# Kernel optimization log

Measured on AMD Instinct MI355X. Metric: run time of the kernel, lower is better.

The kernel has to match this reference:

```python
import jax, jax.numpy as jnp
import numpy as np
import math

D_MODEL = 1024
NUM_HEADS = 16  # scale = sqrt(D_MODEL / NUM_HEADS)
BATCH, SEQ = 4, 4096


def setup_inputs() -> dict:
    key = jax.random.key(0)
    ks = jax.random.split(key, 7)
    s = 1.0 / math.sqrt(D_MODEL)
    return {
        "query": jax.random.normal(ks[0], (BATCH, SEQ, D_MODEL), jnp.float32),
        "value": jax.random.normal(ks[1], (BATCH, SEQ, D_MODEL), jnp.float32),
        "Wq": jax.random.normal(ks[2], (D_MODEL, D_MODEL), jnp.float32) * s,
        "bq": jax.random.normal(ks[3], (D_MODEL,), jnp.float32) * s,
        "qk_b": jnp.zeros((D_MODEL,), jnp.float32),
        "Wv": jax.random.normal(ks[4], (D_MODEL, D_MODEL), jnp.float32) * s,
        "bv": jax.random.normal(ks[5], (D_MODEL,), jnp.float32) * s,
    }


def reference(query, value, Wq, bq, qk_b, Wv, bv):
    # q_proj = Linear(query) + extra bias qk_b ; v_proj = Linear(value)
    q = jnp.einsum("bsd,ed->bse", query, Wq) + bq + qk_b   # [B,S,D]
    v = jnp.einsum("bsd,ed->bse", value, Wv) + bv          # [B,S,D]
    inv_scale = math.sqrt(query.shape[-1] / NUM_HEADS)
    scores = jnp.einsum("bqd,bkd->bqk", q, v) / inv_scale  # [B,S,S]
    attn = jax.nn.softmax(scores, axis=-1)
    # dropout_p = 0.0 -> identity
    return jnp.einsum("bqk,bkd->bqd", attn, v)             # [B,S,D]
```

## Files before the change

kernel.cpp:

```cpp
#include <hip/hip_runtime.h>

#define B_ 4
#define S_ 4096
#define D_ 1024

typedef __bf16 bf16;
typedef _Float16 f16;
typedef __attribute__((ext_vector_type(8))) __bf16 bf16x8;
typedef __attribute__((ext_vector_type(8))) _Float16 f16x8;
typedef __attribute__((ext_vector_type(4))) float floatx4;

__device__ inline floatx4 mfma16(bf16x8 a, bf16x8 b, floatx4 c) {
    return __builtin_amdgcn_mfma_f32_16x16x32_bf16(a, b, c, 0, 0, 0);
}
__device__ inline floatx4 mfma_any(bf16x8 a, bf16x8 b, floatx4 c) {
    return __builtin_amdgcn_mfma_f32_16x16x32_bf16(a, b, c, 0, 0, 0);
}
__device__ inline floatx4 mfma_any(f16x8 a, f16x8 b, floatx4 c) {
    return __builtin_amdgcn_mfma_f32_16x16x32_f16(a, b, c, 0, 0, 0);
}

template <typename T> struct vec8_of;
template <> struct vec8_of<bf16> { using type = bf16x8; };
template <> struct vec8_of<f16>  { using type = f16x8; };

__device__ inline bf16x8 cvt8(float4 a, float4 b) {
    bf16x8 h;
    h[0] = (bf16)a.x; h[1] = (bf16)a.y; h[2] = (bf16)a.z; h[3] = (bf16)a.w;
    h[4] = (bf16)b.x; h[5] = (bf16)b.y; h[6] = (bf16)b.z; h[7] = (bf16)b.w;
    return h;
}

__global__ __launch_bounds__(256) void cast_f32_bf16(
    const float* __restrict__ in, bf16* __restrict__ out)
{
    size_t i = ((size_t)blockIdx.x * 256 + threadIdx.x) * 8;
    float4 a = *(const float4*)(in + i);
    float4 b = *(const float4*)(in + i + 4);
    *(bf16x8*)(out + i) = cvt8(a, b);
}

template <typename TI, typename TO, bool HAS_BIAS>
__global__ __launch_bounds__(512, 2) void gemm256(
    const TI* __restrict__ A, const TI* __restrict__ B, TO* __restrict__ C,
    int K, int ldc, size_t strideA, size_t strideB, size_t strideC,
    const float* __restrict__ bias1, const float* __restrict__ bias2,
    float scale, int tiles_n)
{
    using v8 = typename vec8_of<TI>::type;
    __shared__ __align__(16) TI sA[2][2][8192];
    __shared__ __align__(16) TI sB[2][2][8192];

    A += (size_t)blockIdx.z * strideA;
    B += (size_t)blockIdx.z * strideB;
    C += (size_t)blockIdx.z * strideC;

    const int tid = threadIdx.x;
    const int wave = tid >> 6, lane = tid & 63, quad = lane >> 4, l16 = lane & 15;
    const int wm = wave >> 2, wn = wave & 3;

    const int gx = gridDim.x;
    const int cpx = gx >> 3;
    const int lid = (blockIdx.x & 7) * cpx + (blockIdx.x >> 3);
    const int tm = lid / tiles_n, tn = lid - tm * tiles_n;
    const int m0 = tm * 256, n0 = tn * 256;

    int r_[2], c_[2];
#pragma unroll
    for (int j = 0; j < 2; j++) {
        int idx = j * 512 + tid;
        int dB = idx * 16;
        int L = dB ^ (((dB >> 7) & 7) << 4);
        r_[j] = L >> 7;
        c_[j] = (L & 127) >> 1;
    }
    const int NT = K >> 6;

    auto stageA = [&](int t, int half, int bufsel) {
#pragma unroll
        for (int j = 0; j < 2; j++) {
            int idx = j * 512 + tid;
            __builtin_amdgcn_global_load_lds(
                (const __attribute__((address_space(1))) void*)(
                    A + (size_t)(m0 + half * 128 + r_[j]) * K + t * 64 + c_[j]),
                (__attribute__((address_space(3))) void*)(sA[bufsel][half] + idx * 8),
                16, 0, 0);
        }
    };
    auto stageB = [&](int t, int half, int bufsel) {
#pragma unroll
        for (int j = 0; j < 2; j++) {
            int idx = j * 512 + tid;
            __builtin_amdgcn_global_load_lds(
                (const __attribute__((address_space(1))) void*)(
                    B + (size_t)(n0 + half * 128 + r_[j]) * K + t * 64 + c_[j]),
                (__attribute__((address_space(3))) void*)(sB[bufsel][half] + idx * 8),
                16, 0, 0);
        }
    };
    auto rdA = [&](int buf, int i, int q) -> v8 {
        int row = i * 16 + l16;
        int byte = (row * 128 + q * 64 + quad * 16) ^ ((row & 7) << 4);
        return *(const v8*)((const char*)(sA[buf][wm]) + byte);
    };
    auto rdB = [&](int buf, int j, int q) -> v8 {
        int row = (wn & 1) * 64 + j * 16 + l16;
        int byte = (row * 128 + q * 64 + quad * 16) ^ ((row & 7) << 4);
        return *(const v8*)((const char*)(sB[buf][wn >> 1]) + byte);
    };

    floatx4 acc[8][4];
#pragma unroll
    for (int i = 0; i < 8; i++)
#pragma unroll
        for (int j = 0; j < 4; j++) acc[i][j] = (floatx4)0.0f;

    {
        int t1 = (1 < NT) ? 1 : NT - 1;
        stageA(0, 0, 0); stageA(0, 1, 0);
        stageB(0, 0, 0); stageB(0, 1, 0);
        stageB(t1, 0, 1); stageB(t1, 1, 1);
        asm volatile("s_waitcnt vmcnt(4)" ::: "memory");
        __builtin_amdgcn_s_barrier();
    }

    v8 a[8], b0[4], b1[4];
    for (int t = 0; t < NT; t++) {
        const int buf = t & 1;
        const int tA = (t + 1 < NT) ? t + 1 : NT - 1;
        const int tB = (t + 2 < NT) ? t + 2 : NT - 1;

#pragma unroll
        for (int i = 0; i < 4; i++) { a[2 * i] = rdA(buf, i, 0); a[2 * i + 1] = rdA(buf, i, 1); }
#pragma unroll
        for (int j = 0; j < 2; j++) { b0[2 * j] = rdB(buf, j, 0); b0[2 * j + 1] = rdB(buf, j, 1); }
        stageA(tA, 0, buf ^ 1);
        __builtin_amdgcn_s_barrier();
        __builtin_amdgcn_s_setprio(1);
#pragma unroll
        for (int i = 0; i < 4; i++)
#pragma unroll
            for (int j = 0; j < 2; j++) {
                acc[i][j] = mfma_any(a[2 * i], b0[2 * j], acc[i][j]);
                acc[i][j] = mfma_any(a[2 * i + 1], b0[2 * j + 1], acc[i][j]);
            }
        __builtin_amdgcn_s_setprio(0);
        __builtin_amdgcn_s_barrier();

#pragma unroll
        for (int j = 0; j < 2; j++) { b1[2 * j] = rdB(buf, 2 + j, 0); b1[2 * j + 1] = rdB(buf, 2 + j, 1); }
        stageA(tA, 1, buf ^ 1);
        __builtin_amdgcn_s_barrier();
        __builtin_amdgcn_s_setprio(1);
#pragma unroll
        for (int i = 0; i < 4; i++)
#pragma unroll
            for (int j = 0; j < 2; j++) {
                acc[i][2 + j] = mfma_any(a[2 * i], b1[2 * j], acc[i][2 + j]);
                acc[i][2 + j] = mfma_any(a[2 * i + 1], b1[2 * j + 1], acc[i][2 + j]);
            }
        __builtin_amdgcn_s_setprio(0);
        __builtin_amdgcn_s_barrier();

#pragma unroll
        for (int i = 0; i < 4; i++) { a[2 * i] = rdA(buf, 4 + i, 0); a[2 * i + 1] = rdA(buf, 4 + i, 1); }
        stageB(tB, 0, buf);
        __builtin_amdgcn_s_barrier();
        __builtin_amdgcn_s_setprio(1);
#pragma unroll
        for (int i = 0; i < 4; i++)
#pragma unroll
            for (int j = 0; j < 2; j++) {
                acc[4 + i][2 + j] = mfma_any(a[2 * i], b1[2 * j], acc[4 + i][2 + j]);
                acc[4 + i][2 + j] = mfma_any(a[2 * i + 1], b1[2 * j + 1], acc[4 + i][2 + j]);
            }
        __builtin_amdgcn_s_setprio(0);
        __builtin_amdgcn_s_barrier();

        stageB(tB, 1, buf);
        asm volatile("s_waitcnt vmcnt(4)" ::: "memory");
        __builtin_amdgcn_s_barrier();
        __builtin_amdgcn_s_setprio(1);
#pragma unroll
        for (int i = 0; i < 4; i++)
#pragma unroll
            for (int j = 0; j < 2; j++) {
                acc[4 + i][j] = mfma_any(a[2 * i], b0[2 * j], acc[4 + i][j]);
                acc[4 + i][j] = mfma_any(a[2 * i + 1], b0[2 * j + 1], acc[4 + i][j]);
            }
        __builtin_amdgcn_s_setprio(0);
        __builtin_amdgcn_s_barrier();
    }

#pragma unroll
    for (int mf = 0; mf < 8; mf++)
#pragma unroll
        for (int nf = 0; nf < 4; nf++) {
            int col = n0 + wn * 64 + nf * 16 + l16;
            float badd = 0.0f;
            if (HAS_BIAS) {
                badd = bias1[col];
                if (bias2) badd += bias2[col];
            }
#pragma unroll
            for (int r = 0; r < 4; r++) {
                int row = m0 + wm * 128 + mf * 16 + quad * 4 + r;
                float v = acc[mf][nf][r];
                if (HAS_BIAS) v = (v + badd) * scale;
                C[(size_t)row * ldc + col] = (TO)v;
            }
        }
}

template <typename TI, typename TO, bool HAS_BIAS>
__global__ __launch_bounds__(256) void gemm128(
    const TI* __restrict__ A, const TI* __restrict__ B, TO* __restrict__ C,
    int K, int ldc, size_t strideA, size_t strideB, size_t strideC,
    const float* __restrict__ bias1, const float* __restrict__ bias2, float scale)
{
    using v8 = typename vec8_of<TI>::type;
    __shared__ TI sA[2 * 128 * 32];
    __shared__ TI sB[2 * 128 * 32];
    A += (size_t)blockIdx.z * strideA;
    B += (size_t)blockIdx.z * strideB;
    C += (size_t)blockIdx.z * strideC;

    const int tid = threadIdx.x;
    const int wave = tid >> 6, lane = tid & 63, quad = lane >> 4, l16 = lane & 15;
    const int m0 = blockIdx.x * 128, n0 = blockIdx.y * 128;
    const int wr = (wave >> 1) * 64, wc = (wave & 1) * 64;

    floatx4 acc[4][4];
#pragma unroll
    for (int i = 0; i < 4; i++)
#pragma unroll
        for (int j = 0; j < 4; j++) acc[i][j] = (floatx4)0.0f;

    for (int k0 = 0; k0 < K; k0 += 64) {
#pragma unroll
        for (int s = 0; s < 2; s++) {
#pragma unroll
            for (int j = 0; j < 2; j++) {
                int idx = j * 256 + tid;
                int r = idx >> 2, c = (idx & 3) * 8;
                __builtin_amdgcn_global_load_lds(
                    (const __attribute__((address_space(1))) void*)(A + (size_t)(m0 + r) * K + k0 + s * 32 + c),
                    (__attribute__((address_space(3))) void*)(sA + s * 4096 + idx * 8), 16, 0, 0);
                __builtin_amdgcn_global_load_lds(
                    (const __attribute__((address_space(1))) void*)(B + (size_t)(n0 + r) * K + k0 + s * 32 + c),
                    (__attribute__((address_space(3))) void*)(sB + s * 4096 + idx * 8), 16, 0, 0);
            }
        }
        __syncthreads();
#pragma unroll
        for (int s = 0; s < 2; s++) {
            v8 af[4], bfv[4];
#pragma unroll
            for (int i = 0; i < 4; i++) {
                af[i]  = *(const v8*)&sA[s * 4096 + (wr + i * 16 + l16) * 32 + quad * 8];
                bfv[i] = *(const v8*)&sB[s * 4096 + (wc + i * 16 + l16) * 32 + quad * 8];
            }
#pragma unroll
            for (int mf = 0; mf < 4; mf++)
#pragma unroll
                for (int nf = 0; nf < 4; nf++)
                    acc[mf][nf] = mfma_any(af[mf], bfv[nf], acc[mf][nf]);
        }
        __syncthreads();
    }

#pragma unroll
    for (int mf = 0; mf < 4; mf++)
#pragma unroll
        for (int nf = 0; nf < 4; nf++) {
            int col = n0 + wc + nf * 16 + l16;
            float badd = 0.0f;
            if (HAS_BIAS) {
                badd = bias1[col];
                if (bias2) badd += bias2[col];
            }
#pragma unroll
            for (int r = 0; r < 4; r++) {
                int row = m0 + wr + mf * 16 + quad * 4 + r;
                float v = acc[mf][nf][r];
                if (HAS_BIAS) v = (v + badd) * scale;
                C[(size_t)row * ldc + col] = (TO)v;
            }
        }
}

__global__ __launch_bounds__(256) void transpose_v(
    const bf16* __restrict__ vb, bf16* __restrict__ vtb)
{
    __shared__ bf16 tile[32][33];
    const int b = blockIdx.z;
    const int s0 = blockIdx.x * 32, d0 = blockIdx.y * 32;
    const int tr = threadIdx.x >> 5;
    const int tc = threadIdx.x & 31;
#pragma unroll
    for (int k = 0; k < 4; k++) {
        int r = tr + k * 8;
        tile[r][tc] = vb[((size_t)b * S_ + s0 + r) * D_ + d0 + tc];
    }
    __syncthreads();
#pragma unroll
    for (int k = 0; k < 4; k++) {
        int r = tr + k * 8;
        vtb[((size_t)b * D_ + d0 + r) * S_ + s0 + tc] = tile[tc][r];
    }
}

__global__ __launch_bounds__(256) void transpose_v_f16(
    const bf16* __restrict__ vb, f16* __restrict__ vtb)
{
    __shared__ bf16 tile[32][33];
    const int b = blockIdx.z;
    const int s0 = blockIdx.x * 32, d0 = blockIdx.y * 32;
    const int tr = threadIdx.x >> 5;
    const int tc = threadIdx.x & 31;
#pragma unroll
    for (int k = 0; k < 4; k++) {
        int r = tr + k * 8;
        tile[r][tc] = vb[((size_t)b * S_ + s0 + r) * D_ + d0 + tc];
    }
    __syncthreads();
#pragma unroll
    for (int k = 0; k < 4; k++) {
        int r = tr + k * 8;
        vtb[((size_t)b * D_ + d0 + r) * S_ + s0 + tc] = (f16)(float)tile[tc][r];
    }
}

__global__ __launch_bounds__(256) void softmax_inplace_f16(f16* __restrict__ Sc)
{
    f16* row = Sc + (size_t)blockIdx.x * S_;
    const int tid = threadIdx.x, wave = tid >> 6, lane = tid & 63;
    __shared__ float redm[4], redl[4];

    f16x8 a = *(const f16x8*)(row + tid * 16);
    f16x8 b = *(const f16x8*)(row + tid * 16 + 8);
    float v[16];
#pragma unroll
    for (int j = 0; j < 8; j++) { v[j] = (float)a[j]; v[8 + j] = (float)b[j]; }

    float m = -1e30f;
#pragma unroll
    for (int j = 0; j < 16; j++) m = fmaxf(m, v[j]);
#pragma unroll
    for (int off = 32; off; off >>= 1) m = fmaxf(m, __shfl_xor(m, off));
    if (lane == 0) redm[wave] = m;
    __syncthreads();
    m = fmaxf(fmaxf(redm[0], redm[1]), fmaxf(redm[2], redm[3]));

    float s = 0.0f;
#pragma unroll
    for (int j = 0; j < 16; j++) { v[j] = __expf(v[j] - m); s += v[j]; }
#pragma unroll
    for (int off = 32; off; off >>= 1) s += __shfl_xor(s, off);
    if (lane == 0) redl[wave] = s;
    __syncthreads();
    s = redl[0] + redl[1] + redl[2] + redl[3];
    float inv = 1.0f / s;

#pragma unroll
    for (int j = 0; j < 8; j++) { a[j] = (f16)(v[j] * inv); b[j] = (f16)(v[8 + j] * inv); }
    *(f16x8*)(row + tid * 16) = a;
    *(f16x8*)(row + tid * 16 + 8) = b;
}

__global__ __launch_bounds__(256) void softmax_row(
    const float* __restrict__ Sc, f16* __restrict__ P)
{
    const int q = blockIdx.x;
    const float* row = Sc + (size_t)q * S_;
    f16* prow = P + (size_t)q * S_;
    const int tid = threadIdx.x, wave = tid >> 6, lane = tid & 63;

    float4 v[4];
#pragma unroll
    for (int i = 0; i < 4; i++) v[i] = *(const float4*)(row + tid * 16 + i * 4);

    float m = -1e30f;
#pragma unroll
    for (int i = 0; i < 4; i++)
        m = fmaxf(m, fmaxf(fmaxf(v[i].x, v[i].y), fmaxf(v[i].z, v[i].w)));
#pragma unroll
    for (int off = 32; off; off >>= 1) m = fmaxf(m, __shfl_xor(m, off));
    __shared__ float redm[4], redl[4];
    if (lane == 0) redm[wave] = m;
    __syncthreads();
    m = fmaxf(fmaxf(redm[0], redm[1]), fmaxf(redm[2], redm[3]));

    float p[16];
    float s = 0.0f;
#pragma unroll
    for (int i = 0; i < 4; i++) {
        p[i * 4 + 0] = __expf(v[i].x - m);
        p[i * 4 + 1] = __expf(v[i].y - m);
        p[i * 4 + 2] = __expf(v[i].z - m);
        p[i * 4 + 3] = __expf(v[i].w - m);
        s += p[i * 4] + p[i * 4 + 1] + p[i * 4 + 2] + p[i * 4 + 3];
    }
#pragma unroll
    for (int off = 32; off; off >>= 1) s += __shfl_xor(s, off);
    if (lane == 0) redl[wave] = s;
    __syncthreads();
    s = redl[0] + redl[1] + redl[2] + redl[3];
    float inv = 1.0f / s;

    f16x8 o0, o1;
#pragma unroll
    for (int j = 0; j < 8; j++) {
        o0[j] = (f16)(p[j] * inv);
        o1[j] = (f16)(p[8 + j] * inv);
    }
    *(f16x8*)(prow + tid * 16) = o0;
    *(f16x8*)(prow + tid * 16 + 8) = o1;
}

#define SSTR 40
__global__ __launch_bounds__(256) void proj_gemm(
    const float* __restrict__ A, const float* __restrict__ W,
    const float* __restrict__ bias1, const float* __restrict__ bias2,
    bf16* __restrict__ C, float scale)
{
    __shared__ bf16 sA[64 * SSTR];
    __shared__ bf16 sB[64 * SSTR];
    const int tid = threadIdx.x;
    const int wave = tid >> 6, lane = tid & 63, quad = lane >> 4, l16 = lane & 15;
    const int m0 = blockIdx.x * 64, n0 = blockIdx.y * 64;
    const int wr = (wave >> 1) * 32, wc = (wave & 1) * 32;
    const int lr = tid >> 2;
    const int lc = (tid & 3) * 8;

    floatx4 acc[2][2];
#pragma unroll
    for (int i = 0; i < 2; i++)
#pragma unroll
        for (int j = 0; j < 2; j++) acc[i][j] = (floatx4)0.0f;

    for (int k0 = 0; k0 < 1024; k0 += 32) {
        const float* ga = A + (size_t)(m0 + lr) * 1024 + k0 + lc;
        const float* gw = W + (size_t)(n0 + lr) * 1024 + k0 + lc;
        float4 a0 = *(const float4*)ga;
        float4 a1 = *(const float4*)(ga + 4);
        float4 w0 = *(const float4*)gw;
        float4 w1 = *(const float4*)(gw + 4);
        *(bf16x8*)&sA[lr * SSTR + lc] = cvt8(a0, a1);
        *(bf16x8*)&sB[lr * SSTR + lc] = cvt8(w0, w1);
        __syncthreads();
        bf16x8 af[2], bfv[2];
        af[0]  = *(bf16x8*)&sA[(wr + l16) * SSTR + quad * 8];
        af[1]  = *(bf16x8*)&sA[(wr + 16 + l16) * SSTR + quad * 8];
        bfv[0] = *(bf16x8*)&sB[(wc + l16) * SSTR + quad * 8];
        bfv[1] = *(bf16x8*)&sB[(wc + 16 + l16) * SSTR + quad * 8];
#pragma unroll
        for (int mf = 0; mf < 2; mf++)
#pragma unroll
            for (int nf = 0; nf < 2; nf++)
                acc[mf][nf] = mfma16(af[mf], bfv[nf], acc[mf][nf]);
        __syncthreads();
    }
#pragma unroll
    for (int mf = 0; mf < 2; mf++)
#pragma unroll
        for (int nf = 0; nf < 2; nf++) {
            int col = n0 + wc + nf * 16 + l16;
            float bsum = bias1[col] + (bias2 ? bias2[col] : 0.0f);
#pragma unroll
            for (int r = 0; r < 4; r++) {
                int row = m0 + wr + mf * 16 + quad * 4 + r;
                C[(size_t)row * 1024 + col] = (bf16)((acc[mf][nf][r] + bsum) * scale);
            }
        }
}

#define BR 32
#define TK 64
#define DC 256
__global__ __launch_bounds__(256, 2) void flash_attn(
    const bf16* __restrict__ qb, const bf16* __restrict__ vb,
    const bf16* __restrict__ vtb, float* __restrict__ out)
{
    __shared__ float sPart[4][32][65];
    __shared__ bf16 sP[32][72];
    __shared__ float sM[32], sL[32], sAlpha[32];

    const int tid = threadIdx.x;
    const int wave = tid >> 6, lane = tid & 63, quad = lane >> 4, l16 = lane & 15;
    const int b = blockIdx.y, q0 = blockIdx.x * BR;

    bf16x8 qf[2][8];
#pragma unroll
    for (int mf = 0; mf < 2; mf++)
#pragma unroll
        for (int ks = 0; ks < 8; ks++) {
            int row = q0 + mf * 16 + l16;
            int col = wave * DC + ks * 32 + quad * 8;
            qf[mf][ks] = *(const bf16x8*)(qb + ((size_t)b * S_ + row) * D_ + col);
        }

    floatx4 o[2][16];
#pragma unroll
    for (int mf = 0; mf < 2; mf++)
#pragma unroll
        for (int nf = 0; nf < 16; nf++) o[mf][nf] = (floatx4)0.0f;

    if (tid < 32) { sM[tid] = -1e30f; sL[tid] = 0.0f; }
    __syncthreads();

    for (int kt = 0; kt < S_ / TK; kt++) {
        const int k0 = kt * TK;
        floatx4 sp[2][4];
#pragma unroll
        for (int mf = 0; mf < 2; mf++)
#pragma unroll
            for (int nf = 0; nf < 4; nf++) sp[mf][nf] = (floatx4)0.0f;
#pragma unroll
        for (int ks = 0; ks < 8; ks++) {
            int col = wave * DC + ks * 32 + quad * 8;
#pragma unroll
            for (int nf = 0; nf < 4; nf++) {
                int key = k0 + nf * 16 + l16;
                bf16x8 vf = *(const bf16x8*)(vb + ((size_t)b * S_ + key) * D_ + col);
                sp[0][nf] = mfma16(qf[0][ks], vf, sp[0][nf]);
                sp[1][nf] = mfma16(qf[1][ks], vf, sp[1][nf]);
            }
        }
#pragma unroll
        for (int mf = 0; mf < 2; mf++)
#pragma unroll
            for (int nf = 0; nf < 4; nf++)
#pragma unroll
                for (int r = 0; r < 4; r++)
                    sPart[wave][mf * 16 + quad * 4 + r][nf * 16 + l16] = sp[mf][nf][r];
        __syncthreads();

        {
            const int rr = tid >> 3, c0 = (tid & 7) * 8;
            float v[8];
            float mx = -1e30f;
#pragma unroll
            for (int j = 0; j < 8; j++) {
                v[j] = sPart[0][rr][c0 + j] + sPart[1][rr][c0 + j] +
                       sPart[2][rr][c0 + j] + sPart[3][rr][c0 + j];
                mx = fmaxf(mx, v[j]);
            }
            mx = fmaxf(mx, __shfl_xor(mx, 1));
            mx = fmaxf(mx, __shfl_xor(mx, 2));
            mx = fmaxf(mx, __shfl_xor(mx, 4));
            float m_old = sM[rr];
            float m_new = fmaxf(m_old, mx);
            float rsum = 0.0f;
#pragma unroll
            for (int j = 0; j < 8; j++) {
                float p = __expf(v[j] - m_new);
                sP[rr][c0 + j] = (bf16)p;
                rsum += p;
            }
            rsum += __shfl_xor(rsum, 1);
            rsum += __shfl_xor(rsum, 2);
            rsum += __shfl_xor(rsum, 4);
            if ((tid & 7) == 0) {
                float alpha = __expf(m_old - m_new);
                sAlpha[rr] = alpha;
                sM[rr] = m_new;
                sL[rr] = sL[rr] * alpha + rsum;
            }
        }
        __syncthreads();

        float al[2][4];
#pragma unroll
        for (int mf = 0; mf < 2; mf++)
#pragma unroll
            for (int r = 0; r < 4; r++) al[mf][r] = sAlpha[mf * 16 + quad * 4 + r];
#pragma unroll
        for (int mf = 0; mf < 2; mf++)
#pragma unroll
            for (int nf = 0; nf < 16; nf++)
#pragma unroll
                for (int r = 0; r < 4; r++) o[mf][nf][r] *= al[mf][r];

#pragma unroll
        for (int ks2 = 0; ks2 < 2; ks2++) {
            bf16x8 pA[2];
            pA[0] = *(bf16x8*)&sP[l16][ks2 * 32 + quad * 8];
            pA[1] = *(bf16x8*)&sP[16 + l16][ks2 * 32 + quad * 8];
            int key = k0 + ks2 * 32 + quad * 8;
#pragma unroll
            for (int nf = 0; nf < 16; nf++) {
                int d = wave * DC + nf * 16 + l16;
                bf16x8 vtf = *(const bf16x8*)(vtb + ((size_t)b * D_ + d) * S_ + key);
                o[0][nf] = mfma16(pA[0], vtf, o[0][nf]);
                o[1][nf] = mfma16(pA[1], vtf, o[1][nf]);
            }
        }
        __syncthreads();
    }

#pragma unroll
    for (int mf = 0; mf < 2; mf++) {
        float inv[4];
#pragma unroll
        for (int r = 0; r < 4; r++) inv[r] = 1.0f / sL[mf * 16 + quad * 4 + r];
#pragma unroll
        for (int nf = 0; nf < 16; nf++) {
            int d = wave * DC + nf * 16 + l16;
#pragma unroll
            for (int r = 0; r < 4; r++) {
                int row = q0 + mf * 16 + quad * 4 + r;
                out[((size_t)b * S_ + row) * D_ + d] = o[mf][nf][r] * inv[r];
            }
        }
    }
}

extern "C" void kernel_launch(void* const* d_in, const int* in_sizes, int n_in,
                              void* d_out, int out_size, void* d_ws, size_t ws_size,
                              hipStream_t stream) {
    const float* query = (const float*)d_in[0];
    const float* value = (const float*)d_in[1];
    const float* Wq    = (const float*)d_in[2];
    const float* bq    = (const float*)d_in[3];
    const float* qk_b  = (const float*)d_in[4];
    const float* Wv    = (const float*)d_in[5];
    const float* bv    = (const float*)d_in[6];
    float* out = (float*)d_out;

    const size_t SD = (size_t)S_ * D_;
    const size_t SS = (size_t)S_ * S_;
    const size_t MB = 1024 * 1024;

    char* w = (char*)d_ws;
    bf16* qb = (bf16*)w;
    bf16* vb = (bf16*)(w + 32 * MB);

    if (ws_size >= 224 * MB) {
        f16* vtb = (f16*)(w + 64 * MB);
        f16* Sc  = (f16*)(w + 96 * MB);
        bf16* qc  = (bf16*)(w + 96 * MB);
        bf16* vc  = (bf16*)(w + 128 * MB);
        bf16* wqc = (bf16*)(w + 160 * MB);
        bf16* wvc = (bf16*)(w + 163 * MB);

        cast_f32_bf16<<<(B_ * SD) / 2048, 256, 0, stream>>>(query, qc);
        cast_f32_bf16<<<(B_ * SD) / 2048, 256, 0, stream>>>(value, vc);
        cast_f32_bf16<<<((size_t)D_ * D_) / 2048, 256, 0, stream>>>(Wq, wqc);
        cast_f32_bf16<<<((size_t)D_ * D_) / 2048, 256, 0, stream>>>(Wv, wvc);

        gemm256<bf16, bf16, true><<<dim3(256, 1, 1), 512, 0, stream>>>(
            qc, wqc, qb, D_, D_, 0, 0, 0, bq, qk_b, 0.125f, 4);
        gemm256<bf16, bf16, true><<<dim3(256, 1, 1), 512, 0, stream>>>(
            vc, wvc, vb, D_, D_, 0, 0, 0, bv, nullptr, 1.0f, 4);

        transpose_v_f16<<<dim3(S_ / 32, D_ / 32, B_), 256, 0, stream>>>(vb, vtb);

        gemm256<bf16, f16, false><<<dim3(256, 1, B_), 512, 0, stream>>>(
            qb, vb, Sc, D_, S_, SD, SD, SS, nullptr, nullptr, 1.0f, 16);

        softmax_inplace_f16<<<B_ * S_, 256, 0, stream>>>(Sc);

        gemm256<f16, float, false><<<dim3(64, 1, B_), 512, 0, stream>>>(
            Sc, vtb, out, S_, D_, SS, (size_t)D_ * S_, SD, nullptr, nullptr, 1.0f, 4);
    } else if (ws_size >= 192 * MB) {
        f16*   vtb = (f16*)(w + 64 * MB);
        float* Sc  = (float*)(w + 96 * MB);
        f16*   Pn  = (f16*)(w + 160 * MB);
        bf16*  qc  = (bf16*)(w + 96 * MB);
        bf16*  vc  = (bf16*)(w + 128 * MB);
        bf16*  wqc = (bf16*)(w + 160 * MB);
        bf16*  wvc = (bf16*)(w + 163 * MB);

        cast_f32_bf16<<<(B_ * SD) / 2048, 256, 0, stream>>>(query, qc);
        cast_f32_bf16<<<(B_ * SD) / 2048, 256, 0, stream>>>(value, vc);
        cast_f32_bf16<<<((size_t)D_ * D_) / 2048, 256, 0, stream>>>(Wq, wqc);
        cast_f32_bf16<<<((size_t)D_ * D_) / 2048, 256, 0, stream>>>(Wv, wvc);

        gemm128<bf16, bf16, true><<<dim3(128, 8, 1), 256, 0, stream>>>(
            qc, wqc, qb, D_, D_, 0, 0, 0, bq, qk_b, 0.125f);
        gemm128<bf16, bf16, true><<<dim3(128, 8, 1), 256, 0, stream>>>(
            vc, wvc, vb, D_, D_, 0, 0, 0, bv, nullptr, 1.0f);

        transpose_v_f16<<<dim3(S_ / 32, D_ / 32, B_), 256, 0, stream>>>(vb, vtb);

        for (int b = 0; b < B_; b++) {
            gemm128<bf16, float, false><<<dim3(32, 32, 1), 256, 0, stream>>>(
                qb + b * SD, vb + b * SD, Sc, D_, S_, 0, 0, 0, nullptr, nullptr, 1.0f);
            softmax_row<<<S_, 256, 0, stream>>>(Sc, Pn);
            gemm128<f16, float, false><<<dim3(32, 8, 1), 256, 0, stream>>>(
                Pn, vtb + (size_t)b * D_ * S_, out + b * SD, S_, D_,
                0, 0, 0, nullptr, nullptr, 1.0f);
        }
    } else {
        bf16* vtb = (bf16*)(w + 64 * MB);
        dim3 pg(16384 / 64, 1024 / 64);
        proj_gemm<<<pg, 256, 0, stream>>>(query, Wq, bq, qk_b, qb, 0.125f);
        proj_gemm<<<pg, 256, 0, stream>>>(value, Wv, bv, nullptr, vb, 1.0f);
        transpose_v<<<dim3(S_ / 32, D_ / 32, B_), 256, 0, stream>>>(vb, vtb);
        flash_attn<<<dim3(S_ / BR, B_), 256, 0, stream>>>(qb, vb, vtb, out);
    }
}
```

Measured before the change: 587.2 us.

## Restructure GEMM mainloop to prefetch next-tile fragments and group tiles 4x4

Reorders the 256x256 GEMM main loop so that A and B fragments for the next K-tile are read from shared memory while the current tile's MFMAs run. A is now staged two tiles ahead and B one tile ahead, with separate register sets (A0/A1, BP/BC) and adjusted vmcnt waits. It also remaps block IDs into 4x4 super-tiles for better L2 reuse and precomputes global base offsets to cut address arithmetic. The extra fragment registers raise register pressure, and the finer wait counts make correctness depend on precise load ordering.

```diff
diff --git a/kernel.cpp b/kernel.cpp
--- a/kernel.cpp
+++ b/kernel.cpp
@@ -62,19 +62,27 @@
     const int gx = gridDim.x;
     const int cpx = gx >> 3;
     const int lid = (blockIdx.x & 7) * cpx + (blockIdx.x >> 3);
-    const int tm = lid / tiles_n, tn = lid - tm * tiles_n;
+    const int p = lid >> 4, w = lid & 15;
+    const int pr = tiles_n >> 2;
+    const int Pm = p / pr, Pn = p - Pm * pr;
+    const int tm = Pm * 4 + (w >> 2), tn = Pn * 4 + (w & 3);
     const int m0 = tm * 256, n0 = tn * 256;
 
-    int r_[2], c_[2];
+    const TI* Abase = A + (size_t)m0 * K;
+    const TI* Bbase = B + (size_t)n0 * K;
+
+    size_t goff[2];
 #pragma unroll
     for (int j = 0; j < 2; j++) {
         int idx = j * 512 + tid;
         int dB = idx * 16;
         int L = dB ^ (((dB >> 7) & 7) << 4);
-        r_[j] = L >> 7;
-        c_[j] = (L & 127) >> 1;
+        int r = L >> 7;
+        int c = (L & 127) >> 1;
+        goff[j] = (size_t)r * K + c;
     }
     const int NT = K >> 6;
+    const size_t halfA = (size_t)128 * K;
 
     auto stageA = [&](int t, int half, int bufsel) {
 #pragma unroll
@@ -82,7 +90,7 @@
             int idx = j * 512 + tid;
             __builtin_amdgcn_global_load_lds(
                 (const __attribute__((address_space(1))) void*)(
-                    A + (size_t)(m0 + half * 128 + r_[j]) * K + t * 64 + c_[j]),
+                    Abase + (size_t)t * 64 + (half ? halfA : 0) + goff[j]),
                 (__attribute__((address_space(3))) void*)(sA[bufsel][half] + idx * 8),
                 16, 0, 0);
         }
@@ -93,7 +101,7 @@
             int idx = j * 512 + tid;
             __builtin_amdgcn_global_load_lds(
                 (const __attribute__((address_space(1))) void*)(
-                    B + (size_t)(n0 + half * 128 + r_[j]) * K + t * 64 + c_[j]),
+                    Bbase + (size_t)t * 64 + (half ? halfA : 0) + goff[j]),
                 (__attribute__((address_space(3))) void*)(sB[bufsel][half] + idx * 8),
                 16, 0, 0);
         }
@@ -119,74 +127,80 @@
         int t1 = (1 < NT) ? 1 : NT - 1;
         stageA(0, 0, 0); stageA(0, 1, 0);
         stageB(0, 0, 0); stageB(0, 1, 0);
-        stageB(t1, 0, 1); stageB(t1, 1, 1);
+        stageA(t1, 0, 1); stageA(t1, 1, 1);
         asm volatile("s_waitcnt vmcnt(4)" ::: "memory");
         __builtin_amdgcn_s_barrier();
     }
 
-    v8 a[8], b0[4], b1[4];
+    v8 A0[8], A1[8], BP[4], BC[4];
+#pragma unroll
+    for (int i = 0; i < 4; i++) { A0[2 * i] = rdA(0, i, 0); A0[2 * i + 1] = rdA(0, i, 1); }
+#pragma unroll
+    for (int j = 0; j < 2; j++) { BP[2 * j] = rdB(0, j, 0); BP[2 * j + 1] = rdB(0, j, 1); }
+
     for (int t = 0; t < NT; t++) {
         const int buf = t & 1;
-        const int tA = (t + 1 < NT) ? t + 1 : NT - 1;
-        const int tB = (t + 2 < NT) ? t + 2 : NT - 1;
-
-#pragma unroll
-        for (int i = 0; i < 4; i++) { a[2 * i] = rdA(buf, i, 0); a[2 * i + 1] = rdA(buf, i, 1); }
-#pragma unroll
-        for (int j = 0; j < 2; j++) { b0[2 * j] = rdB(buf, j, 0); b0[2 * j + 1] = rdB(buf, j, 1); }
-        stageA(tA, 0, buf ^ 1);
+        const int tB = (t + 1 < NT) ? t + 1 : NT - 1;
+        const int tA2 = (t + 2 < NT) ? t + 2 : NT - 1;
+
+#pragma unroll
+        for (int j = 0; j < 2; j++) { BC[2 * j] = rdB(buf, 2 + j, 0); BC[2 * j + 1] = rdB(buf, 2 + j, 1); }
+        stageB(tB, 0, buf ^ 1);
         __builtin_amdgcn_s_barrier();
         __builtin_amdgcn_s_setprio(1);
 #pragma unroll
         for (int i = 0; i < 4; i++)
 #pragma unroll
             for (int j = 0; j < 2; j++) {
-                acc[i][j] = mfma_any(a[2 * i], b0[2 * j], acc[i][j]);
-                acc[i][j] = mfma_any(a[2 * i + 1], b0[2 * j + 1], acc[i][j]);
+                acc[i][j] = mfma_any(A0[2 * i], BP[2 * j], acc[i][j]);
+                acc[i][j] = mfma_any(A0[2 * i + 1], BP[2 * j + 1], acc[i][j]);
             }
         __builtin_amdgcn_s_setprio(0);
         __builtin_amdgcn_s_barrier();
 
 #pragma unroll
-        for (int j = 0; j < 2; j++) { b1[2 * j] = rdB(buf, 2 + j, 0); b1[2 * j + 1] = rdB(buf, 2 + j, 1); }
-        stageA(tA, 1, buf ^ 1);
+        for (int i = 0; i < 4; i++) { A1[2 * i] = rdA(buf, 4 + i, 0); A1[2 * i + 1] = rdA(buf, 4 + i, 1); }
+        stageB(tB, 1, buf ^ 1);
         __builtin_amdgcn_s_barrier();
         __builtin_amdgcn_s_setprio(1);
 #pragma unroll
         for (int i = 0; i < 4; i++)
 #pragma unroll
             for (int j = 0; j < 2; j++) {
-                acc[i][2 + j] = mfma_any(a[2 * i], b1[2 * j], acc[i][2 + j]);
-                acc[i][2 + j] = mfma_any(a[2 * i + 1], b1[2 * j + 1], acc[i][2 + j]);
+                acc[i][2 + j] = mfma_any(A0[2 * i], BC[2 * j], acc[i][2 + j]);
+                acc[i][2 + j] = mfma_any(A0[2 * i + 1], BC[2 * j + 1], acc[i][2 + j]);
             }
         __builtin_amdgcn_s_setprio(0);
-        __builtin_amdgcn_s_barrier();
-
-#pragma unroll
-        for (int i = 0; i < 4; i++) { a[2 * i] = rdA(buf, 4 + i, 0); a[2 * i + 1] = rdA(buf, 4 + i, 1); }
-        stageB(tB, 0, buf);
+        asm volatile("s_waitcnt vmcnt(4)" ::: "memory");
+        __builtin_amdgcn_s_barrier();
+
+#pragma unroll
+        for (int i = 0; i < 4; i++) { A0[2 * i] = rdA(buf ^ 1, i, 0); A0[2 * i + 1] = rdA(buf ^ 1, i, 1); }
+        stageA(tA2, 0, buf);
         __builtin_amdgcn_s_barrier();
         __builtin_amdgcn_s_setprio(1);
 #pragma unroll
         for (int i = 0; i < 4; i++)
 #pragma unroll
             for (int j = 0; j < 2; j++) {
-                acc[4 + i][2 + j] = mfma_any(a[2 * i], b1[2 * j], acc[4 + i][2 + j]);
-                acc[4 + i][2 + j] = mfma_any(a[2 * i + 1], b1[2 * j + 1], acc[4 + i][2 + j]);
+                acc[4 + i][j] = mfma_any(A1[2 * i], BP[2 * j], acc[4 + i][j]);
+                acc[4 + i][j] = mfma_any(A1[2 * i + 1], BP[2 * j + 1], acc[4 + i][j]);
             }
         __builtin_amdgcn_s_setprio(0);
-        __builtin_amdgcn_s_barrier();
-
-        stageB(tB, 1, buf);
-        asm volatile("s_waitcnt vmcnt(4)" ::: "memory");
+        asm volatile("s_waitcnt vmcnt(2)" ::: "memory");
+        __builtin_amdgcn_s_barrier();
+
+#pragma unroll
+        for (int j = 0; j < 2; j++) { BP[2 * j] = rdB(buf ^ 1, j, 0); BP[2 * j + 1] = rdB(buf ^ 1, j, 1); }
+        stageA(tA2, 1, buf);
         __builtin_amdgcn_s_barrier();
         __builtin_amdgcn_s_setprio(1);
 #pragma unroll
         for (int i = 0; i < 4; i++)
 #pragma unroll
             for (int j = 0; j < 2; j++) {
-                acc[4 + i][j] = mfma_any(a[2 * i], b0[2 * j], acc[4 + i][j]);
-                acc[4 + i][j] = mfma_any(a[2 * i + 1], b0[2 * j + 1], acc[4 + i][j]);
+                acc[4 + i][2 + j] = mfma_any(A1[2 * i], BC[2 * j], acc[4 + i][2 + j]);
+                acc[4 + i][2 + j] = mfma_any(A1[2 * i + 1], BC[2 * j + 1], acc[4 + i][2 + j]);
             }
         __builtin_amdgcn_s_setprio(0);
         __builtin_amdgcn_s_barrier();
```

Result: slower. 633.1 us (+7.8%).
